# Optimization experiments

Hardware: AMD Instinct MI355X
Metric: run time of the kernel (lower is better)

The kernel has to match this reference:

```python
import jax, jax.numpy as jnp
import numpy as np

B, T, D = 4, 2048, 2048
H, DK, DV = 16, 128, 128


def setup_inputs() -> dict:
    key = jax.random.key(0)
    ks = jax.random.split(key, 8)
    s = 1.0 / np.sqrt(D)
    return {
        "q": jax.random.normal(ks[0], (B, T, D), jnp.float32),
        "k": jax.random.normal(ks[1], (B, T, D), jnp.float32),
        "v": jax.random.normal(ks[2], (B, T, D), jnp.float32),
        "mask": jnp.tril(jnp.ones((T, T), dtype=bool)),  # True = attend
        # weights stored as [in, out] (torch Linear applies x @ W.T)
        "Wq": jax.random.normal(ks[3], (D, H * DK), jnp.float32) * s,
        "Wk": jax.random.normal(ks[4], (D, H * DK), jnp.float32) * s,
        "Wv": jax.random.normal(ks[5], (D, H * DV), jnp.float32) * s,
        "Wo": jax.random.normal(ks[6], (H * DV, D), jnp.float32) * s,
    }


def _attention(q, k, v, mask, Wq, Wk, Wv, Wo):
    # project and split heads: [B,T,H*dh] -> [B,H,T,dh]
    def split_heads(x, dh):
        b, t, _ = x.shape
        return x.reshape(b, t, H, dh).transpose(0, 2, 1, 3)

    q_i = split_heads(q @ Wq, DK)
    k_i = split_heads(k @ Wk, DK)
    v_i = split_heads(v @ Wv, DV)

    scores = jnp.einsum("bhik,bhjk->bhij", q_i, k_i) / jnp.sqrt(
        jnp.asarray(DK, q_i.dtype)
    )
    neg = -jnp.finfo(scores.dtype).max
    scores = jnp.where(mask[None, None, :, :], scores, neg)
    attn = jax.nn.softmax(scores, axis=-1)
    vals = jnp.einsum("bhij,bhjv->bhiv", attn, v_i)  # [B,H,T,dv]
    merged = vals.transpose(0, 2, 1, 3).reshape(q.shape[0], q.shape[1], H * DV)
    return merged @ Wo


def reference(q, k, v, mask, Wq, Wk, Wv, Wo):
    return _attention(q, k, v, mask, Wq, Wk, Wv, Wo)
```

## Files before the change

### kernel.cpp

```cpp
#include <hip/hip_runtime.h>
#include <hip/hip_bf16.h>

typedef __attribute__((ext_vector_type(8))) short bf16x8;
typedef __attribute__((ext_vector_type(4))) unsigned short u16x4;
typedef __attribute__((ext_vector_type(4))) float f32x4;

constexpr int Bb = 4, Tt = 2048, Dd = 2048, Hh = 16, DHd = 128;

static __device__ __forceinline__ unsigned short f2bf(float f) {
  union { float f; unsigned u; } x; x.f = f;
  unsigned r = x.u + 0x7fffu + ((x.u >> 16) & 1u);
  return (unsigned short)(r >> 16);
}

static __device__ __forceinline__ void gld16(const void* g, void* l) {
  __builtin_amdgcn_global_load_lds(
      (__attribute__((address_space(1))) void*)g,
      (__attribute__((address_space(3))) void*)l, 16, 0, 0);
}

__global__ __launch_bounds__(256) void cvt_bf16(const float* __restrict__ s,
                                                unsigned short* __restrict__ d) {
  const size_t i = ((size_t)blockIdx.x * 256 + threadIdx.x) * 8;
  float4 a = *(const float4*)(s + i);
  float4 b = *(const float4*)(s + i + 4);
  bf16x8 pk;
  pk[0] = (short)f2bf(a.x); pk[1] = (short)f2bf(a.y);
  pk[2] = (short)f2bf(a.z); pk[3] = (short)f2bf(a.w);
  pk[4] = (short)f2bf(b.x); pk[5] = (short)f2bf(b.y);
  pk[6] = (short)f2bf(b.z); pk[7] = (short)f2bf(b.w);
  *(bf16x8*)(d + i) = pk;
}

__global__ __launch_bounds__(256) void wtrans_all(
    const float* __restrict__ Wq, const float* __restrict__ Wk,
    const float* __restrict__ Wv, const float* __restrict__ Wo,
    unsigned short* __restrict__ WqT, unsigned short* __restrict__ WkT,
    unsigned short* __restrict__ WvT, unsigned short* __restrict__ WoT,
    float qscale) {
  __shared__ __align__(16) unsigned short tile[64][72];
  const float* src;
  unsigned short* dst;
  float sc = 1.0f;
  switch (blockIdx.z) {
    case 0: src = Wq; dst = WqT; sc = qscale; break;
    case 1: src = Wk; dst = WkT; break;
    case 2: src = Wv; dst = WvT; break;
    default: src = Wo; dst = WoT; break;
  }
  const int t = threadIdx.x;
  const int k0 = blockIdx.x * 64, n0 = blockIdx.y * 64;
  const int c = t & 15, r = t >> 4;
#pragma unroll
  for (int p = 0; p < 4; ++p) {
    const int rr = r + 16 * p;
    float4 v = *(const float4*)(src + (size_t)(k0 + rr) * Dd + n0 + c * 4);
    u16x4 pk;
    pk[0] = f2bf(v.x * sc); pk[1] = f2bf(v.y * sc);
    pk[2] = f2bf(v.z * sc); pk[3] = f2bf(v.w * sc);
    *(u16x4*)&tile[rr][c * 4] = pk;
  }
  __syncthreads();
#pragma unroll
  for (int p = 0; p < 4; ++p) {
    const int nn = r + 16 * p;
    u16x4 pk;
    pk[0] = tile[c * 4 + 0][nn]; pk[1] = tile[c * 4 + 1][nn];
    pk[2] = tile[c * 4 + 2][nn]; pk[3] = tile[c * 4 + 3][nn];
    *(u16x4*)(dst + (size_t)(n0 + nn) * Dd + k0 + c * 4) = pk;
  }
}

template <int OMODE>
__global__ __launch_bounds__(512, 2) void gemm8p(
    const unsigned short* __restrict__ A, const unsigned short* __restrict__ Bt,
    void* __restrict__ Outp) {
  __shared__ __align__(16) unsigned short As[2][2][128 * 64];
  __shared__ __align__(16) unsigned short Bs[2][2][128 * 64];
  const int t = threadIdx.x, lane = t & 63, w = t >> 6;
  const int wm = w >> 2, wn = w & 3;
  const int fr = lane & 15, fq = lane >> 4;
  const int sw = fr & 7;
  const int slot = blockIdx.x;
  const int orig = (slot & 7) * 32 + (slot >> 3);
  const int m0 = (orig >> 3) * 256, n0 = (orig & 7) * 256;

  const int srow = t >> 3, sch = t & 7;
  const int scol = (sch ^ (srow & 7)) * 8;

  auto SA = [&](int tau, int h) {
    const unsigned short* g =
        A + (size_t)(m0 + h * 128 + srow) * Dd + tau * 64 + scol;
    unsigned short* l = &As[tau & 1][h][(srow * 8 + sch) * 8];
    gld16(g, l);
    gld16(g + (size_t)64 * Dd, l + 4096);
  };
  auto SB = [&](int tau, int h) {
    const unsigned short* g =
        Bt + (size_t)(n0 + h * 128 + srow) * Dd + tau * 64 + scol;
    unsigned short* l = &Bs[tau & 1][h][(srow * 8 + sch) * 8];
    gld16(g, l);
    gld16(g + (size_t)64 * Dd, l + 4096);
  };

  f32x4 acc[8][4] = {};
  constexpr int NT = Dd / 64;

  SB(0, 0); SB(0, 1); SA(0, 0); SA(0, 1);
  SB(1, 0); SB(1, 1); SA(1, 0); SA(1, 1);
  asm volatile("s_waitcnt vmcnt(8)" ::: "memory");
  __builtin_amdgcn_s_barrier();
  __builtin_amdgcn_sched_barrier(0);

  for (int tau = 0; tau < NT; ++tau) {
    const unsigned short* Ab = &As[tau & 1][wm][0];
    const unsigned short* Bb = &Bs[tau & 1][wn >> 1][0];
    const int brow = (wn & 1) * 64;

    bf16x8 a0[4][2], a1[4][2], b0[2][2], b1[2][2];

#pragma unroll
    for (int i = 0; i < 4; ++i)
#pragma unroll
      for (int ks = 0; ks < 2; ++ks)
        a0[i][ks] = *(const bf16x8*)&Ab[(i * 16 + fr) * 64 +
                                        (((ks * 4 + fq) ^ sw)) * 8];
#pragma unroll
    for (int j = 0; j < 2; ++j)
#pragma unroll
      for (int ks = 0; ks < 2; ++ks)
        b0[j][ks] = *(const bf16x8*)&Bb[(brow + j * 16 + fr) * 64 +
                                        (((ks * 4 + fq) ^ sw)) * 8];
    __builtin_amdgcn_s_barrier();
    __builtin_amdgcn_sched_barrier(0);
    __builtin_amdgcn_s_setprio(1);
#pragma unroll
    for (int i = 0; i < 4; ++i)
#pragma unroll
      for (int j = 0; j < 2; ++j)
#pragma unroll
        for (int ks = 0; ks < 2; ++ks)
          acc[i][j] = __builtin_amdgcn_mfma_f32_16x16x32_bf16(
              a0[i][ks], b0[j][ks], acc[i][j], 0, 0, 0);
    __builtin_amdgcn_s_setprio(0);
    __builtin_amdgcn_sched_barrier(0);
    __builtin_amdgcn_s_barrier();

#pragma unroll
    for (int j = 0; j < 2; ++j)
#pragma unroll
      for (int ks = 0; ks < 2; ++ks)
        b1[j][ks] = *(const bf16x8*)&Bb[(brow + (j + 2) * 16 + fr) * 64 +
                                        (((ks * 4 + fq) ^ sw)) * 8];
    __builtin_amdgcn_s_barrier();
    __builtin_amdgcn_sched_barrier(0);
    __builtin_amdgcn_s_setprio(1);
#pragma unroll
    for (int i = 0; i < 4; ++i)
#pragma unroll
      for (int j = 0; j < 2; ++j)
#pragma unroll
        for (int ks = 0; ks < 2; ++ks)
          acc[i][j + 2] = __builtin_amdgcn_mfma_f32_16x16x32_bf16(
              a0[i][ks], b1[j][ks], acc[i][j + 2], 0, 0, 0);
    __builtin_amdgcn_s_setprio(0);
    __builtin_amdgcn_sched_barrier(0);
    __builtin_amdgcn_s_barrier();

#pragma unroll
    for (int i = 0; i < 4; ++i)
#pragma unroll
      for (int ks = 0; ks < 2; ++ks)
        a1[i][ks] = *(const bf16x8*)&Ab[((i + 4) * 16 + fr) * 64 +
                                        (((ks * 4 + fq) ^ sw)) * 8];
    if (tau + 2 < NT) {
      SB(tau + 2, 0);
      SB(tau + 2, 1);
    }
    __builtin_amdgcn_s_barrier();
    __builtin_amdgcn_sched_barrier(0);
    __builtin_amdgcn_s_setprio(1);
#pragma unroll
    for (int i = 0; i < 4; ++i)
#pragma unroll
      for (int j = 0; j < 2; ++j)
#pragma unroll
        for (int ks = 0; ks < 2; ++ks)
          acc[i + 4][j] = __builtin_amdgcn_mfma_f32_16x16x32_bf16(
              a1[i][ks], b0[j][ks], acc[i + 4][j], 0, 0, 0);
    __builtin_amdgcn_s_setprio(0);
    __builtin_amdgcn_sched_barrier(0);
    __builtin_amdgcn_s_barrier();

    if (tau + 2 < NT) {
      SA(tau + 2, 0);
      SA(tau + 2, 1);
      asm volatile("s_waitcnt vmcnt(8)" ::: "memory");
    } else {
      asm volatile("s_waitcnt vmcnt(0)" ::: "memory");
    }
    __builtin_amdgcn_s_barrier();
    __builtin_amdgcn_sched_barrier(0);
    __builtin_amdgcn_s_setprio(1);
#pragma unroll
    for (int i = 0; i < 4; ++i)
#pragma unroll
      for (int j = 0; j < 2; ++j)
#pragma unroll
        for (int ks = 0; ks < 2; ++ks)
          acc[i + 4][j + 2] = __builtin_amdgcn_mfma_f32_16x16x32_bf16(
              a1[i][ks], b1[j][ks], acc[i + 4][j + 2], 0, 0, 0);
    __builtin_amdgcn_s_setprio(0);
    __builtin_amdgcn_sched_barrier(0);
    __builtin_amdgcn_s_barrier();
  }

#pragma unroll
  for (int m = 0; m < 8; ++m) {
    const int mg = m0 + wm * 128 + m * 16 + fq * 4;
    const int bb = mg >> 11, tt0 = mg & (Tt - 1);
#pragma unroll
    for (int n = 0; n < 4; ++n) {
      const int ng = n0 + wn * 64 + n * 16 + fr;
      if (OMODE == 0) {
        float* o = (float*)Outp + (size_t)mg * Dd + ng;
#pragma unroll
        for (int r = 0; r < 4; ++r) o[(size_t)r * Dd] = acc[m][n][r];
      } else if (OMODE == 1) {
        const int h = ng >> 7, dh = ng & 127;
        unsigned short* o = (unsigned short*)Outp +
                            (((size_t)bb * Hh + h) * Tt + tt0) * DHd + dh;
#pragma unroll
        for (int r = 0; r < 4; ++r) o[r * DHd] = f2bf(acc[m][n][r]);
      } else {
        const int h = ng >> 7, dh = ng & 127;
        u16x4 pk;
#pragma unroll
        for (int r = 0; r < 4; ++r) pk[r] = f2bf(acc[m][n][r]);
        *(u16x4*)((unsigned short*)Outp +
                  (((size_t)bb * Hh + h) * DHd + dh) * Tt + tt0) = pk;
      }
    }
  }
}

__global__ __launch_bounds__(512, 2) void fattn(
    const unsigned short* __restrict__ Qp, const unsigned short* __restrict__ Kp,
    const unsigned short* __restrict__ Vt, unsigned short* __restrict__ Ao) {
  __shared__ __align__(16) unsigned short Ks[2][64 * 128];
  __shared__ __align__(16) unsigned short Vs[2][128 * 64];
  const int t = threadIdx.x, lane = t & 63, w = t >> 6;
  const int fr = lane & 15, fq = lane >> 4;
  const int rsw = fr & 7;
  const int id = blockIdx.x;
  const int xcd = id & 7, slot = id >> 3;
  const int s5 = slot >> 5, r_ = slot & 31;
  const int bh = xcd * 8 + (r_ >> 2);
  const int q2 = r_ & 3;
  const int qb = s5 ? q2 : 7 - q2;
  const int q0w = qb * 256 + w * 32;
  const unsigned short* Qb = Qp + (size_t)bh * Tt * DHd;
  const unsigned short* Kb = Kp + (size_t)bh * Tt * DHd;
  const unsigned short* Vb = Vt + (size_t)bh * DHd * Tt;

  bf16x8 qf[2][4];
#pragma unroll
  for (int mg = 0; mg < 2; ++mg)
#pragma unroll
    for (int ks = 0; ks < 4; ++ks)
      qf[mg][ks] = *(const bf16x8*)(Qb + (size_t)(q0w + mg * 16 + fr) * DHd +
                                    ks * 32 + fq * 8);

  f32x4 oacc[2][8] = {};
  float m_[2] = {-1e30f, -1e30f};
  float l_[2] = {0.f, 0.f};

  auto STAGE = [&](int b, int kv0) {
#pragma unroll
    for (int p = 0; p < 2; ++p) {
      const int idx = t + p * 512, row = idx >> 4, ch = idx & 15;
      gld16(Kb + (size_t)(kv0 + row) * DHd + ((ch ^ (row & 7)) * 8),
            &Ks[b][idx * 8]);
    }
#pragma unroll
    for (int p = 0; p < 2; ++p) {
      const int idx = t + p * 512, row = idx >> 3, ch = idx & 7;
      gld16(Vb + (size_t)row * Tt + kv0 + ((ch ^ (row & 7)) * 8),
            &Vs[b][idx * 8]);
    }
  };

  const int ntile = 4 * qb + 4;
  STAGE(0, 0);
  asm volatile("s_waitcnt vmcnt(0)" ::: "memory");
  int cur = 0;

  for (int kt = 0; kt < ntile; ++kt) {
    const int kv0 = kt * 64;
    __builtin_amdgcn_s_barrier();
    if (kt + 1 < ntile) STAGE(cur ^ 1, (kt + 1) * 64);
    __builtin_amdgcn_sched_barrier(0);

    if (kv0 <= q0w + 31) {
      const unsigned short* Kc = &Ks[cur][0];
      const unsigned short* Vc = &Vs[cur][0];

      f32x4 s[2][4] = {};
      __builtin_amdgcn_s_setprio(1);
#pragma unroll
      for (int tt = 0; tt < 4; ++tt) {
        bf16x8 kf[4];
#pragma unroll
        for (int ks = 0; ks < 4; ++ks)
          kf[ks] = *(const bf16x8*)(Kc + (tt * 16 + fr) * 128 +
                                    ((ks * 4 + fq) ^ rsw) * 8);
#pragma unroll
        for (int ks = 0; ks < 4; ++ks) {
          s[0][tt] = __builtin_amdgcn_mfma_f32_16x16x32_bf16(kf[ks], qf[0][ks],
                                                             s[0][tt], 0, 0, 0);
          s[1][tt] = __builtin_amdgcn_mfma_f32_16x16x32_bf16(kf[ks], qf[1][ks],
                                                             s[1][tt], 0, 0, 0);
        }
      }
      __builtin_amdgcn_s_setprio(0);

      uint2 c[2][4];
#pragma unroll
      for (int mg = 0; mg < 2; ++mg) {
        const int qg = q0w + mg * 16;
        if (kv0 + 63 > qg) {
          const int qa = qg + fr;
#pragma unroll
          for (int tt = 0; tt < 4; ++tt)
#pragma unroll
            for (int r = 0; r < 4; ++r)
              if (kv0 + tt * 16 + fq * 4 + r > qa) s[mg][tt][r] = -1e30f;
        }

        float tmax = s[mg][0][0];
#pragma unroll
        for (int tt = 0; tt < 4; ++tt)
#pragma unroll
          for (int r = 0; r < 4; ++r) tmax = fmaxf(tmax, s[mg][tt][r]);
        tmax = fmaxf(tmax, __shfl_xor(tmax, 16));
        tmax = fmaxf(tmax, __shfl_xor(tmax, 32));

        if (!__all(tmax <= m_[mg] + 8.0f)) {
          const float mn = fmaxf(m_[mg], tmax);
          const float alpha = __builtin_amdgcn_exp2f(m_[mg] - mn);
          m_[mg] = mn;
          float al4[4];
#pragma unroll
          for (int r = 0; r < 4; ++r) al4[r] = __shfl(alpha, fq * 4 + r);
#pragma unroll
          for (int dt = 0; dt < 8; ++dt)
#pragma unroll
            for (int r = 0; r < 4; ++r) oacc[mg][dt][r] *= al4[r];
          l_[mg] *= alpha;
        }

        float rs = 0.f;
#pragma unroll
        for (int tt = 0; tt < 4; ++tt)
#pragma unroll
          for (int r = 0; r < 4; ++r) {
            const float p = __builtin_amdgcn_exp2f(s[mg][tt][r] - m_[mg]);
            s[mg][tt][r] = p;
            rs += p;
          }
        rs += __shfl_xor(rs, 16);
        rs += __shfl_xor(rs, 32);
        l_[mg] += rs;

#pragma unroll
        for (int tt = 0; tt < 4; ++tt) {
          unsigned r0, r1;
          asm("v_cvt_pk_bf16_f32 %0, %1, %2"
              : "=v"(r0) : "v"(s[mg][tt][0]), "v"(s[mg][tt][1]));
          asm("v_cvt_pk_bf16_f32 %0, %1, %2"
              : "=v"(r1) : "v"(s[mg][tt][2]), "v"(s[mg][tt][3]));
          c[mg][tt].x = r0; c[mg][tt].y = r1;
        }
      }

      const int src0 = fr + 32 * (fq & 1);
      const int src1 = src0 + 16;
      const bool hi = (fq >> 1) != 0;
      __builtin_amdgcn_s_setprio(1);
#pragma unroll
      for (int ks2 = 0; ks2 < 2; ++ks2) {
        bf16x8 pf[2];
#pragma unroll
        for (int mg = 0; mg < 2; ++mg) {
          const int a0 = __shfl((int)c[mg][2 * ks2].x, src0);
          const int b0 = __shfl((int)c[mg][2 * ks2 + 1].x, src0);
          const int a1 = __shfl((int)c[mg][2 * ks2].y, src0);
          const int b1 = __shfl((int)c[mg][2 * ks2 + 1].y, src0);
          const int a2 = __shfl((int)c[mg][2 * ks2].x, src1);
          const int b2 = __shfl((int)c[mg][2 * ks2 + 1].x, src1);
          const int a3 = __shfl((int)c[mg][2 * ks2].y, src1);
          const int b3 = __shfl((int)c[mg][2 * ks2 + 1].y, src1);
          union { int wd[4]; bf16x8 v; } pu;
          pu.wd[0] = hi ? b0 : a0;
          pu.wd[1] = hi ? b1 : a1;
          pu.wd[2] = hi ? b2 : a2;
          pu.wd[3] = hi ? b3 : a3;
          pf[mg] = pu.v;
        }
#pragma unroll
        for (int dt = 0; dt < 8; ++dt) {
          const bf16x8 vf = *(const bf16x8*)(Vc + (dt * 16 + fr) * 64 +
                                             ((ks2 * 4 + fq) ^ rsw) * 8);
          oacc[0][dt] = __builtin_amdgcn_mfma_f32_16x16x32_bf16(pf[0], vf,
                                                                oacc[0][dt], 0, 0, 0);
          oacc[1][dt] = __builtin_amdgcn_mfma_f32_16x16x32_bf16(pf[1], vf,
                                                                oacc[1][dt], 0, 0, 0);
        }
      }
      __builtin_amdgcn_s_setprio(0);
    }

    if (kt + 1 < ntile)
      asm volatile("s_waitcnt vmcnt(0)" ::: "memory");
    cur ^= 1;
  }

  const int bb = bh >> 4, hh = bh & 15;
#pragma unroll
  for (int mg = 0; mg < 2; ++mg) {
    float linv[4];
#pragma unroll
    for (int r = 0; r < 4; ++r) linv[r] = 1.0f / __shfl(l_[mg], fq * 4 + r);
    const int qrow = q0w + mg * 16 + fq * 4;
#pragma unroll
    for (int r = 0; r < 4; ++r) {
      unsigned short* o = Ao + ((size_t)bb * Tt + qrow + r) * Dd + hh * DHd + fr;
#pragma unroll
      for (int dt = 0; dt < 8; ++dt) o[dt * 16] = f2bf(oacc[mg][dt][r] * linv[r]);
    }
  }
}

extern "C" void kernel_launch(void* const* d_in, const int* in_sizes, int n_in,
                              void* d_out, int out_size, void* d_ws, size_t ws_size,
                              hipStream_t stream) {
  const float* q = (const float*)d_in[0];
  const float* k = (const float*)d_in[1];
  const float* v = (const float*)d_in[2];
  const float* Wq = (const float*)d_in[4];
  const float* Wk = (const float*)d_in[5];
  const float* Wv = (const float*)d_in[6];
  const float* Wo = (const float*)d_in[7];

  const size_t WE = (size_t)Dd * Dd;
  const size_t PE = (size_t)Bb * Hh * Tt * DHd;
  unsigned short* WqT = (unsigned short*)d_ws;
  unsigned short* WkT = WqT + WE;
  unsigned short* WvT = WkT + WE;
  unsigned short* WoT = WvT + WE;
  unsigned short* Qx = WoT + WE;
  unsigned short* Kx = Qx + PE;
  unsigned short* Vx = Kx + PE;
  unsigned short* Ax = Vx + PE;

  const float qscale = (float)(1.4426950408889634 / 11.313708498984761);
  wtrans_all<<<dim3(32, 32, 4), 256, 0, stream>>>(
      Wq, Wk, Wv, Wo, WqT, WkT, WvT, WoT, qscale);

  cvt_bf16<<<dim3(8192), 256, 0, stream>>>(q, Ax);
  gemm8p<1><<<dim3(256), 512, 0, stream>>>(Ax, WqT, Qx);
  cvt_bf16<<<dim3(8192), 256, 0, stream>>>(k, Ax);
  gemm8p<1><<<dim3(256), 512, 0, stream>>>(Ax, WkT, Kx);
  cvt_bf16<<<dim3(8192), 256, 0, stream>>>(v, Ax);
  gemm8p<2><<<dim3(256), 512, 0, stream>>>(Ax, WvT, Vx);
  fattn<<<dim3(512), 512, 0, stream>>>(Qx, Kx, Vx, Ax);
  gemm8p<0><<<dim3(256), 512, 0, stream>>>(Ax, WoT, (float*)d_out);
}
```

Before: 478.9 us.

## Restructure GEMM main loop into two phases with fewer barriers

Reorganizes the projection GEMM inner loop from four quarter-tile MFMA phases into two half-tile phases. All B fragments are loaded once into registers and reused for both A halves. The prefetch loads for the next B and A tiles are issued right after each LDS-read barrier. This cuts the number of workgroup barriers per K step and gives longer MFMA bursts, at the cost of more live registers (bl[4][2]) and a different load/compute interleave.

After: 484.4 us. No clear change (+1.1%).

```diff
diff --git a/kernel.cpp b/kernel.cpp
--- a/kernel.cpp
+++ b/kernel.cpp
@@ -117,7 +117,7 @@
     const unsigned short* Bb = &Bs[tau & 1][wn >> 1][0];
     const int brow = (wn & 1) * 64;
 
-    bf16x8 a0[4][2], a1[4][2], b0[2][2], b1[2][2];
+    bf16x8 a0[4][2], a1[4][2], bl[4][2];
 
 #pragma unroll
     for (int i = 0; i < 4; ++i)
@@ -126,46 +126,30 @@
         a0[i][ks] = *(const bf16x8*)&Ab[(i * 16 + fr) * 64 +
                                         (((ks * 4 + fq) ^ sw)) * 8];
 #pragma unroll
-    for (int j = 0; j < 2; ++j)
+    for (int j = 0; j < 4; ++j)
 #pragma unroll
       for (int ks = 0; ks < 2; ++ks)
-        b0[j][ks] = *(const bf16x8*)&Bb[(brow + j * 16 + fr) * 64 +
+        bl[j][ks] = *(const bf16x8*)&Bb[(brow + j * 16 + fr) * 64 +
                                         (((ks * 4 + fq) ^ sw)) * 8];
+    asm volatile("s_waitcnt lgkmcnt(0)" ::: "memory");
+    __builtin_amdgcn_sched_barrier(0);
     __builtin_amdgcn_s_barrier();
     __builtin_amdgcn_sched_barrier(0);
+    if (tau + 2 < NT) {
+      SB(tau + 2, 0);
+      SB(tau + 2, 1);
+    }
     __builtin_amdgcn_s_setprio(1);
 #pragma unroll
     for (int i = 0; i < 4; ++i)
 #pragma unroll
-      for (int j = 0; j < 2; ++j)
+      for (int j = 0; j < 4; ++j)
 #pragma unroll
         for (int ks = 0; ks < 2; ++ks)
           acc[i][j] = __builtin_amdgcn_mfma_f32_16x16x32_bf16(
-              a0[i][ks], b0[j][ks], acc[i][j], 0, 0, 0);
+              a0[i][ks], bl[j][ks], acc[i][j], 0, 0, 0);
     __builtin_amdgcn_s_setprio(0);
     __builtin_amdgcn_sched_barrier(0);
-    __builtin_amdgcn_s_barrier();
-
-#pragma unroll
-    for (int j = 0; j < 2; ++j)
-#pragma unroll
-      for (int ks = 0; ks < 2; ++ks)
-        b1[j][ks] = *(const bf16x8*)&Bb[(brow + (j + 2) * 16 + fr) * 64 +
-                                        (((ks * 4 + fq) ^ sw)) * 8];
-    __builtin_amdgcn_s_barrier();
-    __builtin_amdgcn_sched_barrier(0);
-    __builtin_amdgcn_s_setprio(1);
-#pragma unroll
-    for (int i = 0; i < 4; ++i)
-#pragma unroll
-      for (int j = 0; j < 2; ++j)
-#pragma unroll
-        for (int ks = 0; ks < 2; ++ks)
-          acc[i][j + 2] = __builtin_amdgcn_mfma_f32_16x16x32_bf16(
-              a0[i][ks], b1[j][ks], acc[i][j + 2], 0, 0, 0);
-    __builtin_amdgcn_s_setprio(0);
-    __builtin_amdgcn_sched_barrier(0);
-    __builtin_amdgcn_s_barrier();
 
 #pragma unroll
     for (int i = 0; i < 4; ++i)
@@ -173,46 +157,32 @@
       for (int ks = 0; ks < 2; ++ks)
         a1[i][ks] = *(const bf16x8*)&Ab[((i + 4) * 16 + fr) * 64 +
                                         (((ks * 4 + fq) ^ sw)) * 8];
-    if (tau + 2 < NT) {
-      SB(tau + 2, 0);
-      SB(tau + 2, 1);
-    }
+    asm volatile("s_waitcnt lgkmcnt(0)" ::: "memory");
+    __builtin_amdgcn_sched_barrier(0);
     __builtin_amdgcn_s_barrier();
     __builtin_amdgcn_sched_barrier(0);
-    __builtin_amdgcn_s_setprio(1);
-#pragma unroll
-    for (int i = 0; i < 4; ++i)
-#pragma unroll
-      for (int j = 0; j < 2; ++j)
-#pragma unroll
-        for (int ks = 0; ks < 2; ++ks)
-          acc[i + 4][j] = __builtin_amdgcn_mfma_f32_16x16x32_bf16(
-              a1[i][ks], b0[j][ks], acc[i + 4][j], 0, 0, 0);
-    __builtin_amdgcn_s_setprio(0);
-    __builtin_amdgcn_sched_barrier(0);
-    __builtin_amdgcn_s_barrier();
-
     if (tau + 2 < NT) {
       SA(tau + 2, 0);
       SA(tau + 2, 1);
+    }
+    __builtin_amdgcn_s_setprio(1);
+#pragma unroll
+    for (int i = 0; i < 4; ++i)
+#pragma unroll
+      for (int j = 0; j < 4; ++j)
+#pragma unroll
+        for (int ks = 0; ks < 2; ++ks)
+          acc[i + 4][j] = __builtin_amdgcn_mfma_f32_16x16x32_bf16(
+              a1[i][ks], bl[j][ks], acc[i + 4][j], 0, 0, 0);
+    __builtin_amdgcn_s_setprio(0);
+    __builtin_amdgcn_sched_barrier(0);
+    if (tau + 2 < NT) {
       asm volatile("s_waitcnt vmcnt(8)" ::: "memory");
-    } else {
+    } else if (tau + 1 < NT) {
       asm volatile("s_waitcnt vmcnt(0)" ::: "memory");
     }
     __builtin_amdgcn_s_barrier();
     __builtin_amdgcn_sched_barrier(0);
-    __builtin_amdgcn_s_setprio(1);
-#pragma unroll
-    for (int i = 0; i < 4; ++i)
-#pragma unroll
-      for (int j = 0; j < 2; ++j)
-#pragma unroll
-        for (int ks = 0; ks < 2; ++ks)
-          acc[i + 4][j + 2] = __builtin_amdgcn_mfma_f32_16x16x32_bf16(
-              a1[i][ks], b1[j][ks], acc[i + 4][j + 2], 0, 0, 0);
-    __builtin_amdgcn_s_setprio(0);
-    __builtin_amdgcn_sched_barrier(0);
-    __builtin_amdgcn_s_barrier();
   }
 
 #pragma unroll
```
